# Optimization experiments

Hardware: AMD Instinct MI355X
Metric: run time of the kernel (lower is better)

## Reference

```python
import jax, jax.numpy as jnp
import numpy as np

N_NODES = 100000
N_EDGES = 1600000
F = 64          # node_features (in == out for EvolveGCNO)
HID = 64        # hidden_size


def setup_inputs() -> dict:
    key = jax.random.key(0)
    ks = jax.random.split(key, 12)
    s = 1.0 / np.sqrt(F)
    inp = {
        "x": jax.random.normal(ks[0], (N_NODES, F), dtype=jnp.float32),
        "edge_index": jax.random.randint(ks[1], (2, N_EDGES), 0, N_NODES, dtype=jnp.int64),
        "edge_weight": jax.random.uniform(ks[2], (N_EDGES,), dtype=jnp.float32),
        # evolving GCN weight (initial_weight of EvolveGCNO)
        "W0": jax.random.uniform(ks[3], (F, F), jnp.float32, -s, s),
        # GRU (input_size=F, hidden_size=F): gates ordered r, z, n
        "gru_Wi": jax.random.uniform(ks[4], (3 * F, F), jnp.float32, -s, s),
        "gru_Wh": jax.random.uniform(ks[5], (3 * F, F), jnp.float32, -s, s),
        "gru_bi": jax.random.uniform(ks[6], (3 * F,), jnp.float32, -s, s),
        "gru_bh": jax.random.uniform(ks[7], (3 * F,), jnp.float32, -s, s),
        # projection F -> HID and head HID -> 1
        "proj_W": jax.random.uniform(ks[8], (HID, F), jnp.float32, -s, s),
        "proj_b": jax.random.uniform(ks[9], (HID,), jnp.float32, -s, s),
        "lin_W": jax.random.uniform(ks[10], (1, HID), jnp.float32, -1.0 / np.sqrt(HID), 1.0 / np.sqrt(HID)),
        "lin_b": jax.random.uniform(ks[11], (1,), jnp.float32, -1.0 / np.sqrt(HID), 1.0 / np.sqrt(HID)),
    }
    return inp


def reference(x, edge_index, edge_weight, W0, gru_Wi, gru_Wh, gru_bi, gru_bh,
              proj_W, proj_b, lin_W, lin_b):
    N = x.shape[0]
    # --- EvolveGCNO weight evolution: one GRU step, rows of W0 are both input and hidden ---
    gi = W0 @ gru_Wi.T + gru_bi  # [F, 3F]
    gh = W0 @ gru_Wh.T + gru_bh  # [F, 3F]
    i_r, i_z, i_n = jnp.split(gi, 3, axis=1)
    h_r, h_z, h_n = jnp.split(gh, 3, axis=1)
    r = jax.nn.sigmoid(i_r + h_r)
    z = jax.nn.sigmoid(i_z + h_z)
    n = jnp.tanh(i_n + r * h_n)
    W = (1.0 - z) * n + z * W0  # evolved GCN weight [F, F]

    # --- GCNConv with fixed evolved W: X' = D^-1/2 (A + I) D^-1/2 (X W) ---
    xw = x @ W  # [N, F]
    src, dst = edge_index[0], edge_index[1]
    loop = jnp.arange(N)
    src2 = jnp.concatenate([src, loop])
    dst2 = jnp.concatenate([dst, loop])
    w2 = jnp.concatenate([edge_weight, jnp.ones((N,), xw.dtype)])  # self-loop weight 1
    deg = jax.ops.segment_sum(w2, dst2, num_segments=N)
    dinv = jnp.where(deg > 0, jax.lax.rsqrt(deg), 0.0)
    norm = dinv[src2] * w2 * dinv[dst2]  # [E + N]
    h = jax.ops.segment_sum(xw[src2] * norm[:, None], dst2, num_segments=N)  # [N, F]

    # --- MLP head (dropout is identity in eval) ---
    h = jax.nn.relu(h @ proj_W.T + proj_b)
    return h @ lin_W.T + lin_b  # [N, 1]
```

## Files before the change

### kernel.cpp

```cpp
#include <hip/hip_runtime.h>
#include <stdint.h>

#define FDIM 64
#define BINSH 6
#define NBINS 1563
#define BCAP 1536
#define OVCAP 8192
#define PSTAGE 8192

__device__ __forceinline__ float bf2f(unsigned int u) {
    union { float f; uint32_t i; } v; v.i = (u & 0xFFFFu) << 16; return v.f;
}
__device__ __forceinline__ unsigned short f2bf(float f) {
    union { float f; uint32_t i; } v; v.f = f;
    uint32_t u = v.i;
    u += 0x7FFFu + ((u >> 16) & 1u);
    return (unsigned short)(u >> 16);
}

__global__ __launch_bounds__(256) void k_sentinel(float* out, int N, float val) {
    int n = blockIdx.x * 256 + threadIdx.x;
    if (n < N) out[n] = (n == 0) ? val : 0.f;
}

__global__ __launch_bounds__(64) void k_evolveM(
    const float* __restrict__ W0, const float* __restrict__ Wi,
    const float* __restrict__ Wh, const float* __restrict__ bi,
    const float* __restrict__ bh, const float* __restrict__ projW,
    float* __restrict__ M, int* __restrict__ gcnt, int* __restrict__ ovf_cnt) {
    int i = blockIdx.x;
    int j = threadIdx.x;
    int g = i * 64 + j;
    if (g < NBINS) gcnt[g] = 0;
    if (g == NBINS) *ovf_cnt = 0;
    __shared__ float w0s[64];
    __shared__ float wrow[64];
    w0s[j] = W0[i * 64 + j];
    __syncthreads();
    float a0 = 0.f, a1 = 0.f, a2 = 0.f, b0 = 0.f, b1 = 0.f, b2 = 0.f;
#pragma unroll 8
    for (int k = 0; k < 64; k++) {
        float w0k = w0s[k];
        a0 += w0k * Wi[(j)       * 64 + k];
        a1 += w0k * Wi[(64 + j)  * 64 + k];
        a2 += w0k * Wi[(128 + j) * 64 + k];
        b0 += w0k * Wh[(j)       * 64 + k];
        b1 += w0k * Wh[(64 + j)  * 64 + k];
        b2 += w0k * Wh[(128 + j) * 64 + k];
    }
    float ir = a0 + bi[j],        hr = b0 + bh[j];
    float iz = a1 + bi[64 + j],   hz = b1 + bh[64 + j];
    float in_ = a2 + bi[128 + j], hn = b2 + bh[128 + j];
    float r = 1.f / (1.f + expf(-(ir + hr)));
    float z = 1.f / (1.f + expf(-(iz + hz)));
    float n = tanhf(in_ + r * hn);
    wrow[j] = (1.f - z) * n + z * w0s[j];
    __syncthreads();
    float s = 0.f;
#pragma unroll 8
    for (int q = 0; q < 64; q++) s += wrow[q] * projW[j * 64 + q];
    M[i * 64 + j] = s;
}

__global__ __launch_bounds__(256) void k_xm(
    const float* __restrict__ x, const float* __restrict__ M,
    unsigned short* __restrict__ xm, int N) {
    __shared__ float xs[64 * 68];
    __shared__ float ms[64 * 68];
    int t  = threadIdx.x;
    int nb = blockIdx.x * 64;
#pragma unroll
    for (int i = 0; i < 4; i++) {
        int lin = i * 1024 + t * 4;
        int row = lin >> 6, col = lin & 63;
        int node = nb + row;
        float4 v = make_float4(0.f, 0.f, 0.f, 0.f);
        if (node < N) v = *(const float4*)(x + (size_t)node * 64 + col);
        *(float4*)&xs[row * 68 + col] = v;
        *(float4*)&ms[row * 68 + col] = *(const float4*)(M + lin);
    }
    __syncthreads();
    int tj = t & 15, tn = t >> 4;
    float acc[4][4] = {};
    for (int k = 0; k < 64; k += 4) {
        float4 xv[4], mv[4];
#pragma unroll
        for (int nn = 0; nn < 4; nn++) xv[nn] = *(const float4*)&xs[(tn * 4 + nn) * 68 + k];
#pragma unroll
        for (int kk = 0; kk < 4; kk++) mv[kk] = *(const float4*)&ms[(k + kk) * 68 + tj * 4];
#pragma unroll
        for (int nn = 0; nn < 4; nn++) {
            const float* xp = (const float*)&xv[nn];
#pragma unroll
            for (int kk = 0; kk < 4; kk++) {
                float xk = xp[kk];
                const float* mp = (const float*)&mv[kk];
                acc[nn][0] += xk * mp[0];
                acc[nn][1] += xk * mp[1];
                acc[nn][2] += xk * mp[2];
                acc[nn][3] += xk * mp[3];
            }
        }
    }
#pragma unroll
    for (int nn = 0; nn < 4; nn++) {
        int node = nb + tn * 4 + nn;
        if (node < N) {
            ushort4 o;
            o.x = f2bf(acc[nn][0]); o.y = f2bf(acc[nn][1]);
            o.z = f2bf(acc[nn][2]); o.w = f2bf(acc[nn][3]);
            *(ushort4*)&xm[(size_t)node * 64 + tj * 4] = o;
        }
    }
}

__global__ __launch_bounds__(1024) void k_part(
    const int* __restrict__ src, const int* __restrict__ dst,
    const float* __restrict__ ew, int* __restrict__ gcnt,
    int2* __restrict__ part, int* __restrict__ ovf_cnt,
    int* __restrict__ ovs, int* __restrict__ ovd, float* __restrict__ ovw,
    int E) {
    __shared__ int hist[NBINS];
    __shared__ int lcur[NBINS];
    int t = threadIdx.x;
    for (int b = t; b < NBINS; b += 1024) hist[b] = 0;
    __syncthreads();
    int e0 = blockIdx.x * PSTAGE;
    int cnt = E - e0; if (cnt > PSTAGE) cnt = PSTAGE;
    for (int i = t; i < cnt; i += 1024) atomicAdd(&hist[dst[e0 + i] >> BINSH], 1);
    __syncthreads();
    for (int b = t; b < NBINS; b += 1024) {
        int h = hist[b];
        lcur[b] = h ? atomicAdd(&gcnt[b], h) : 0;
    }
    __syncthreads();
    for (int i = t; i < cnt; i += 1024) {
        int e = e0 + i;
        int d = dst[e];
        int b = d >> BINSH;
        int p = atomicAdd(&lcur[b], 1);
        if (p < BCAP) {
            part[(size_t)b * BCAP + p] = make_int2(src[e] | ((d & 63) << 20),
                                                   __float_as_int(ew[e]));
        } else {
            int op = atomicAdd(ovf_cnt, 1);
            if (op < OVCAP) {
                ovs[op] = src[e];
                ovd[op] = d;
                ovw[op] = ew[e];
            }
        }
    }
}

__global__ __launch_bounds__(256) void k_deg2(
    const int* __restrict__ gcnt, const int2* __restrict__ part,
    const int* __restrict__ ovf_cnt, const int* __restrict__ ovd,
    const float* __restrict__ ovw,
    float* __restrict__ deg, float* __restrict__ dinv, int N) {
    __shared__ float dl[64];
    int t = threadIdx.x, b = blockIdx.x;
    if (t < 64) dl[t] = 1.0f;
    __syncthreads();
    int c = gcnt[b]; if (c > BCAP) c = BCAP;
    const int2* pe = part + (size_t)b * BCAP;
    for (int i = t; i < c; i += 256) {
        int2 e = pe[i];
        atomicAdd(&dl[(e.x >> 20) & 63], __int_as_float(e.y));
    }
    int m = *ovf_cnt; if (m > OVCAP) m = OVCAP;
    for (int i = t; i < m; i += 256) {
        int d = ovd[i];
        if ((d >> BINSH) == b) atomicAdd(&dl[d & 63], ovw[i]);
    }
    __syncthreads();
    int n = b * 64 + t;
    if (t < 64 && n < N) {
        float d = dl[t];
        deg[n] = d;
        dinv[n] = d > 0.f ? rsqrtf(d) : 0.f;
    }
}

__global__ __launch_bounds__(256) void k_gf(
    const unsigned short* __restrict__ xm, const float* __restrict__ dinv,
    const int* __restrict__ gcnt, const int2* __restrict__ part,
    const float* __restrict__ projB, const float* __restrict__ linW,
    const float* __restrict__ linB, const int* __restrict__ ovf_cnt,
    const int* __restrict__ ovs, const int* __restrict__ ovd,
    const float* __restrict__ ovw, float* __restrict__ out, int N) {
    __shared__ int  lcnt[64];
    __shared__ int  loff[65];
    __shared__ int  lcur[64];
    __shared__ int2 ledge[BCAP];
    __shared__ float pbs[64], lws[64];
    int t = threadIdx.x, b = blockIdx.x;
    if (t < 64) { lcnt[t] = 0; pbs[t] = projB[t]; lws[t] = linW[t]; }
    __syncthreads();
    int c = gcnt[b]; if (c > BCAP) c = BCAP;
    const int2* pe = part + (size_t)b * BCAP;
    for (int i = t; i < c; i += 256) {
        atomicAdd(&lcnt[(pe[i].x >> 20) & 63], 1);
    }
    __syncthreads();
    if (t == 0) {
        int o = 0;
#pragma unroll 16
        for (int k = 0; k < 64; k++) { loff[k] = o; o += lcnt[k]; }
        loff[64] = o;
    }
    __syncthreads();
    if (t < 64) lcur[t] = loff[t];
    __syncthreads();
    for (int i = t; i < c; i += 256) {
        int2 e = pe[i];
        int s = e.x & 0xFFFFF;
        float nw = dinv[s] * __int_as_float(e.y);
        int p = atomicAdd(&lcur[(e.x >> 20) & 63], 1);
        ledge[p] = make_int2(e.x, __float_as_int(nw));
    }
    __syncthreads();
    int m = *ovf_cnt; if (m > OVCAP) m = OVCAP;
    float lb = linB[0];
    int wv = t >> 6, lane = t & 63, eg = lane >> 4, fq = lane & 15, f = fq * 4;
    for (int nl = wv; nl < 64; nl += 4) {
        int n = b * 64 + nl;
        if (n >= N) continue;
        float dn = dinv[n];
        int beg = loff[nl], end = loff[nl + 1];
        float ax = 0.f, ay = 0.f, az = 0.f, aw = 0.f;
        float bx = 0.f, by = 0.f, bz = 0.f, bw = 0.f;
        int i = beg + eg;
        for (; i + 4 < end; i += 8) {
            int2 e0 = ledge[i];
            int2 e1 = ledge[i + 4];
            int s0 = e0.x & 0xFFFFF, s1 = e1.x & 0xFFFFF;
            uint2 u0 = *(const uint2*)&xm[(size_t)s0 * 64 + f];
            uint2 u1 = *(const uint2*)&xm[(size_t)s1 * 64 + f];
            float nm0 = __int_as_float(e0.y);
            float nm1 = __int_as_float(e1.y);
            ax += nm0 * bf2f(u0.x);       ay += nm0 * bf2f(u0.x >> 16);
            az += nm0 * bf2f(u0.y);       aw += nm0 * bf2f(u0.y >> 16);
            bx += nm1 * bf2f(u1.x);       by += nm1 * bf2f(u1.x >> 16);
            bz += nm1 * bf2f(u1.y);       bw += nm1 * bf2f(u1.y >> 16);
        }
        for (; i < end; i += 4) {
            int2 e = ledge[i];
            int s = e.x & 0xFFFFF;
            float nm = __int_as_float(e.y);
            uint2 u = *(const uint2*)&xm[(size_t)s * 64 + f];
            ax += nm * bf2f(u.x); ay += nm * bf2f(u.x >> 16);
            az += nm * bf2f(u.y); aw += nm * bf2f(u.y >> 16);
        }
        ax += bx; ay += by; az += bz; aw += bw;
        ax *= dn; ay *= dn; az *= dn; aw *= dn;
        ax += __shfl_xor(ax, 16); ay += __shfl_xor(ay, 16);
        az += __shfl_xor(az, 16); aw += __shfl_xor(aw, 16);
        ax += __shfl_xor(ax, 32); ay += __shfl_xor(ay, 32);
        az += __shfl_xor(az, 32); aw += __shfl_xor(aw, 32);
        if (eg == 0) {
            {
                uint2 u = *(const uint2*)&xm[(size_t)n * 64 + f];
                float sl = dn * dn;
                ax += sl * bf2f(u.x); ay += sl * bf2f(u.x >> 16);
                az += sl * bf2f(u.y); aw += sl * bf2f(u.y >> 16);
            }
            for (int q = 0; q < m; q++) {
                if (ovd[q] == n) {
                    int s = ovs[q];
                    float nm = dinv[s] * ovw[q] * dn;
                    uint2 u = *(const uint2*)&xm[(size_t)s * 64 + f];
                    ax += nm * bf2f(u.x); ay += nm * bf2f(u.x >> 16);
                    az += nm * bf2f(u.y); aw += nm * bf2f(u.y >> 16);
                }
            }
            float v0 = ax + pbs[f],     v1 = ay + pbs[f + 1];
            float v2 = az + pbs[f + 2], v3 = aw + pbs[f + 3];
            float s = (v0 > 0.f ? v0 : 0.f) * lws[f]
                    + (v1 > 0.f ? v1 : 0.f) * lws[f + 1]
                    + (v2 > 0.f ? v2 : 0.f) * lws[f + 2]
                    + (v3 > 0.f ? v3 : 0.f) * lws[f + 3];
            s += __shfl_xor(s, 1); s += __shfl_xor(s, 2);
            s += __shfl_xor(s, 4); s += __shfl_xor(s, 8);
            if (fq == 0) out[n] = s + lb;
        }
    }
}

extern "C" void kernel_launch(void* const* d_in, const int* in_sizes, int n_in,
                              void* d_out, int out_size, void* d_ws, size_t ws_size,
                              hipStream_t stream) {
    const float* x   = (const float*)d_in[0];
    const int*   ei  = (const int*)d_in[1];
    const float* ew  = (const float*)d_in[2];
    const float* W0  = (const float*)d_in[3];
    const float* gWi = (const float*)d_in[4];
    const float* gWh = (const float*)d_in[5];
    const float* gbi = (const float*)d_in[6];
    const float* gbh = (const float*)d_in[7];
    const float* pW  = (const float*)d_in[8];
    const float* pb  = (const float*)d_in[9];
    const float* lW  = (const float*)d_in[10];
    const float* lb  = (const float*)d_in[11];
    float* out = (float*)d_out;

    static const int EXPSZ[12] = {6400000, 3200000, 1600000, 4096, 12288, 12288,
                                  192, 192, 4096, 64, 64, 1};
    int mism = -1;
    for (int i = 0; i < 12 && i < n_in; i++)
        if (in_sizes[i] != EXPSZ[i]) { mism = i; break; }
    if (mism >= 0) {
        k_sentinel<<<(out_size + 255) / 256, 256, 0, stream>>>(out, out_size,
                                                               ldexpf(1.f, 30 + 3 * mism));
        return;
    }

    int N = in_sizes[0] / FDIM;
    int E = in_sizes[1] / 2;
    const int* src = ei;
    const int* dst = ei + E;

    char* wsb = (char*)d_ws;
    float* M       = (float*)(wsb);
    int*   gcnt    = (int*)  (wsb + (32u << 10));
    int*   ovf_cnt = (int*)  (wsb + (39u << 10));
    int*   ovs     = (int*)  (wsb + (44u << 10));
    int*   ovd     = (int*)  (wsb + (76u << 10));
    float* ovw     = (float*)(wsb + (108u << 10));
    float* deg     = (float*)(wsb + (512u << 10));
    float* dinv    = (float*)(wsb + (1u << 20));
    int2*  part    = (int2*) (wsb + (2u << 20));
    unsigned short* xm = (unsigned short*)(wsb + (22u << 20));

    k_evolveM<<<64, 64, 0, stream>>>(W0, gWi, gWh, gbi, gbh, pW, M, gcnt, ovf_cnt);
    k_xm<<<NBINS, 256, 0, stream>>>(x, M, xm, N);
    k_part<<<(E + PSTAGE - 1) / PSTAGE, 1024, 0, stream>>>(src, dst, ew, gcnt, part,
                                                           ovf_cnt, ovs, ovd, ovw, E);
    k_deg2<<<NBINS, 256, 0, stream>>>(gcnt, part, ovf_cnt, ovd, ovw, deg, dinv, N);
    k_gf<<<NBINS, 256, 0, stream>>>(xm, dinv, gcnt, part, pb, lW, lb,
                                    ovf_cnt, ovs, ovd, ovw, out, N);
}
```

Before: 195.9 us.

## Merge independent kernels into shared launches and precompute per-node edge offsets

Edge partitioning and the GRU weight evolution now run as disjoint block ranges of one launch. The x@M bf16 projection and the degree pass share a second launch the same way. The degree pass also counts edges per node and writes the prefix offsets to global memory, so the gather kernel no longer runs its own histogram and scan. A memset replaces the in-kernel counter zeroing. This cuts five launches down to a memset plus three and removes redundant partition reads, but k_prep's evolve blocks now carry 1024-thread blocks with most threads idle.

After: 193.4 us. No clear change (-1.3%).

```diff
diff --git a/kernel.cpp b/kernel.cpp
--- a/kernel.cpp
+++ b/kernel.cpp
@@ -7,6 +7,8 @@
 #define BCAP 1536
 #define OVCAP 8192
 #define PSTAGE 8192
+#define PBLK 196
+#define LSTRIDE 72
 
 __device__ __forceinline__ float bf2f(unsigned int u) {
     union { float f; uint32_t i; } v; v.i = (u & 0xFFFFu) << 16; return v.f;
@@ -23,195 +25,197 @@
     if (n < N) out[n] = (n == 0) ? val : 0.f;
 }
 
-__global__ __launch_bounds__(64) void k_evolveM(
+__global__ __launch_bounds__(1024) void k_prep(
+    const int* __restrict__ src, const int* __restrict__ dst,
+    const float* __restrict__ ew, int* __restrict__ gcnt,
+    int2* __restrict__ part, int* __restrict__ ovf_cnt,
+    int* __restrict__ ovs, int* __restrict__ ovd, float* __restrict__ ovw, int E,
     const float* __restrict__ W0, const float* __restrict__ Wi,
     const float* __restrict__ Wh, const float* __restrict__ bi,
     const float* __restrict__ bh, const float* __restrict__ projW,
-    float* __restrict__ M, int* __restrict__ gcnt, int* __restrict__ ovf_cnt) {
-    int i = blockIdx.x;
-    int j = threadIdx.x;
-    int g = i * 64 + j;
-    if (g < NBINS) gcnt[g] = 0;
-    if (g == NBINS) *ovf_cnt = 0;
-    __shared__ float w0s[64];
-    __shared__ float wrow[64];
-    w0s[j] = W0[i * 64 + j];
-    __syncthreads();
-    float a0 = 0.f, a1 = 0.f, a2 = 0.f, b0 = 0.f, b1 = 0.f, b2 = 0.f;
+    float* __restrict__ M) {
+    __shared__ char sm[12504];
+    int t = threadIdx.x;
+    if (blockIdx.x < PBLK) {
+        int* hist = (int*)sm;
+        int* lcur = hist + NBINS;
+        for (int b = t; b < NBINS; b += 1024) hist[b] = 0;
+        __syncthreads();
+        int e0 = blockIdx.x * PSTAGE;
+        int cnt = E - e0; if (cnt > PSTAGE) cnt = PSTAGE;
+        for (int i = t; i < cnt; i += 1024) atomicAdd(&hist[dst[e0 + i] >> BINSH], 1);
+        __syncthreads();
+        for (int b = t; b < NBINS; b += 1024) {
+            int h = hist[b];
+            lcur[b] = h ? atomicAdd(&gcnt[b], h) : 0;
+        }
+        __syncthreads();
+        for (int i = t; i < cnt; i += 1024) {
+            int e = e0 + i;
+            int d = dst[e];
+            int b = d >> BINSH;
+            int p = atomicAdd(&lcur[b], 1);
+            if (p < BCAP) {
+                part[(size_t)b * BCAP + p] = make_int2(src[e] | ((d & 63) << 20),
+                                                       __float_as_int(ew[e]));
+            } else {
+                int op = atomicAdd(ovf_cnt, 1);
+                if (op < OVCAP) {
+                    ovs[op] = src[e];
+                    ovd[op] = d;
+                    ovw[op] = ew[e];
+                }
+            }
+        }
+    } else {
+        int i = blockIdx.x - PBLK;
+        float* w0s  = (float*)sm;
+        float* wrow = w0s + 64;
+        if (t < 64) w0s[t] = W0[i * 64 + t];
+        __syncthreads();
+        if (t < 64) {
+            int j = t;
+            float a0 = 0.f, a1 = 0.f, a2 = 0.f, b0 = 0.f, b1 = 0.f, b2 = 0.f;
 #pragma unroll 8
-    for (int k = 0; k < 64; k++) {
-        float w0k = w0s[k];
-        a0 += w0k * Wi[(j)       * 64 + k];
-        a1 += w0k * Wi[(64 + j)  * 64 + k];
-        a2 += w0k * Wi[(128 + j) * 64 + k];
-        b0 += w0k * Wh[(j)       * 64 + k];
-        b1 += w0k * Wh[(64 + j)  * 64 + k];
-        b2 += w0k * Wh[(128 + j) * 64 + k];
-    }
-    float ir = a0 + bi[j],        hr = b0 + bh[j];
-    float iz = a1 + bi[64 + j],   hz = b1 + bh[64 + j];
-    float in_ = a2 + bi[128 + j], hn = b2 + bh[128 + j];
-    float r = 1.f / (1.f + expf(-(ir + hr)));
-    float z = 1.f / (1.f + expf(-(iz + hz)));
-    float n = tanhf(in_ + r * hn);
-    wrow[j] = (1.f - z) * n + z * w0s[j];
-    __syncthreads();
-    float s = 0.f;
+            for (int k = 0; k < 64; k++) {
+                float w0k = w0s[k];
+                a0 += w0k * Wi[(j)       * 64 + k];
+                a1 += w0k * Wi[(64 + j)  * 64 + k];
+                a2 += w0k * Wi[(128 + j) * 64 + k];
+                b0 += w0k * Wh[(j)       * 64 + k];
+                b1 += w0k * Wh[(64 + j)  * 64 + k];
+                b2 += w0k * Wh[(128 + j) * 64 + k];
+            }
+            float ir = a0 + bi[j],        hr = b0 + bh[j];
+            float iz = a1 + bi[64 + j],   hz = b1 + bh[64 + j];
+            float in_ = a2 + bi[128 + j], hn = b2 + bh[128 + j];
+            float r = 1.f / (1.f + expf(-(ir + hr)));
+            float z = 1.f / (1.f + expf(-(iz + hz)));
+            float n = tanhf(in_ + r * hn);
+            wrow[j] = (1.f - z) * n + z * w0s[j];
+        }
+        __syncthreads();
+        if (t < 64) {
+            float s = 0.f;
 #pragma unroll 8
-    for (int q = 0; q < 64; q++) s += wrow[q] * projW[j * 64 + q];
-    M[i * 64 + j] = s;
-}
-
-__global__ __launch_bounds__(256) void k_xm(
+            for (int q = 0; q < 64; q++) s += wrow[q] * projW[t * 64 + q];
+            M[i * 64 + t] = s;
+        }
+    }
+}
+
+__global__ __launch_bounds__(256) void k_xmdeg(
     const float* __restrict__ x, const float* __restrict__ M,
-    unsigned short* __restrict__ xm, int N) {
-    __shared__ float xs[64 * 68];
-    __shared__ float ms[64 * 68];
-    int t  = threadIdx.x;
-    int nb = blockIdx.x * 64;
-#pragma unroll
-    for (int i = 0; i < 4; i++) {
-        int lin = i * 1024 + t * 4;
-        int row = lin >> 6, col = lin & 63;
-        int node = nb + row;
-        float4 v = make_float4(0.f, 0.f, 0.f, 0.f);
-        if (node < N) v = *(const float4*)(x + (size_t)node * 64 + col);
-        *(float4*)&xs[row * 68 + col] = v;
-        *(float4*)&ms[row * 68 + col] = *(const float4*)(M + lin);
-    }
-    __syncthreads();
-    int tj = t & 15, tn = t >> 4;
-    float acc[4][4] = {};
-    for (int k = 0; k < 64; k += 4) {
-        float4 xv[4], mv[4];
-#pragma unroll
-        for (int nn = 0; nn < 4; nn++) xv[nn] = *(const float4*)&xs[(tn * 4 + nn) * 68 + k];
-#pragma unroll
-        for (int kk = 0; kk < 4; kk++) mv[kk] = *(const float4*)&ms[(k + kk) * 68 + tj * 4];
-#pragma unroll
-        for (int nn = 0; nn < 4; nn++) {
-            const float* xp = (const float*)&xv[nn];
-#pragma unroll
-            for (int kk = 0; kk < 4; kk++) {
-                float xk = xp[kk];
-                const float* mp = (const float*)&mv[kk];
-                acc[nn][0] += xk * mp[0];
-                acc[nn][1] += xk * mp[1];
-                acc[nn][2] += xk * mp[2];
-                acc[nn][3] += xk * mp[3];
-            }
-        }
-    }
-#pragma unroll
-    for (int nn = 0; nn < 4; nn++) {
-        int node = nb + tn * 4 + nn;
-        if (node < N) {
-            ushort4 o;
-            o.x = f2bf(acc[nn][0]); o.y = f2bf(acc[nn][1]);
-            o.z = f2bf(acc[nn][2]); o.w = f2bf(acc[nn][3]);
-            *(ushort4*)&xm[(size_t)node * 64 + tj * 4] = o;
-        }
-    }
-}
-
-__global__ __launch_bounds__(1024) void k_part(
-    const int* __restrict__ src, const int* __restrict__ dst,
-    const float* __restrict__ ew, int* __restrict__ gcnt,
-    int2* __restrict__ part, int* __restrict__ ovf_cnt,
-    int* __restrict__ ovs, int* __restrict__ ovd, float* __restrict__ ovw,
-    int E) {
-    __shared__ int hist[NBINS];
-    __shared__ int lcur[NBINS];
-    int t = threadIdx.x;
-    for (int b = t; b < NBINS; b += 1024) hist[b] = 0;
-    __syncthreads();
-    int e0 = blockIdx.x * PSTAGE;
-    int cnt = E - e0; if (cnt > PSTAGE) cnt = PSTAGE;
-    for (int i = t; i < cnt; i += 1024) atomicAdd(&hist[dst[e0 + i] >> BINSH], 1);
-    __syncthreads();
-    for (int b = t; b < NBINS; b += 1024) {
-        int h = hist[b];
-        lcur[b] = h ? atomicAdd(&gcnt[b], h) : 0;
-    }
-    __syncthreads();
-    for (int i = t; i < cnt; i += 1024) {
-        int e = e0 + i;
-        int d = dst[e];
-        int b = d >> BINSH;
-        int p = atomicAdd(&lcur[b], 1);
-        if (p < BCAP) {
-            part[(size_t)b * BCAP + p] = make_int2(src[e] | ((d & 63) << 20),
-                                                   __float_as_int(ew[e]));
-        } else {
-            int op = atomicAdd(ovf_cnt, 1);
-            if (op < OVCAP) {
-                ovs[op] = src[e];
-                ovd[op] = d;
-                ovw[op] = ew[e];
-            }
-        }
-    }
-}
-
-__global__ __launch_bounds__(256) void k_deg2(
+    unsigned short* __restrict__ xm, int N,
     const int* __restrict__ gcnt, const int2* __restrict__ part,
     const int* __restrict__ ovf_cnt, const int* __restrict__ ovd,
-    const float* __restrict__ ovw,
-    float* __restrict__ deg, float* __restrict__ dinv, int N) {
-    __shared__ float dl[64];
-    int t = threadIdx.x, b = blockIdx.x;
-    if (t < 64) dl[t] = 1.0f;
-    __syncthreads();
-    int c = gcnt[b]; if (c > BCAP) c = BCAP;
-    const int2* pe = part + (size_t)b * BCAP;
-    for (int i = t; i < c; i += 256) {
-        int2 e = pe[i];
-        atomicAdd(&dl[(e.x >> 20) & 63], __int_as_float(e.y));
-    }
-    int m = *ovf_cnt; if (m > OVCAP) m = OVCAP;
-    for (int i = t; i < m; i += 256) {
-        int d = ovd[i];
-        if ((d >> BINSH) == b) atomicAdd(&dl[d & 63], ovw[i]);
-    }
-    __syncthreads();
-    int n = b * 64 + t;
-    if (t < 64 && n < N) {
-        float d = dl[t];
-        deg[n] = d;
-        dinv[n] = d > 0.f ? rsqrtf(d) : 0.f;
+    const float* __restrict__ ovw, float* __restrict__ dinv,
+    int* __restrict__ loffg) {
+    __shared__ char sm[34816];
+    int t = threadIdx.x;
+    if (blockIdx.x < NBINS) {
+        float* xs = (float*)sm;
+        float* ms = xs + 64 * 68;
+        int nb = blockIdx.x * 64;
+#pragma unroll
+        for (int i = 0; i < 4; i++) {
+            int lin = i * 1024 + t * 4;
+            int row = lin >> 6, col = lin & 63;
+            int node = nb + row;
+            float4 v = make_float4(0.f, 0.f, 0.f, 0.f);
+            if (node < N) v = *(const float4*)(x + (size_t)node * 64 + col);
+            *(float4*)&xs[row * 68 + col] = v;
+            *(float4*)&ms[row * 68 + col] = *(const float4*)(M + lin);
+        }
+        __syncthreads();
+        int tj = t & 15, tn = t >> 4;
+        float acc[4][4] = {};
+        for (int k = 0; k < 64; k += 4) {
+            float4 xv[4], mv[4];
+#pragma unroll
+            for (int nn = 0; nn < 4; nn++) xv[nn] = *(const float4*)&xs[(tn * 4 + nn) * 68 + k];
+#pragma unroll
+            for (int kk = 0; kk < 4; kk++) mv[kk] = *(const float4*)&ms[(k + kk) * 68 + tj * 4];
+#pragma unroll
+            for (int nn = 0; nn < 4; nn++) {
+                const float* xp = (const float*)&xv[nn];
+#pragma unroll
+                for (int kk = 0; kk < 4; kk++) {
+                    float xk = xp[kk];
+                    const float* mp = (const float*)&mv[kk];
+                    acc[nn][0] += xk * mp[0];
+                    acc[nn][1] += xk * mp[1];
+                    acc[nn][2] += xk * mp[2];
+                    acc[nn][3] += xk * mp[3];
+                }
+            }
+        }
+#pragma unroll
+        for (int nn = 0; nn < 4; nn++) {
+            int node = nb + tn * 4 + nn;
+            if (node < N) {
+                ushort4 o;
+                o.x = f2bf(acc[nn][0]); o.y = f2bf(acc[nn][1]);
+                o.z = f2bf(acc[nn][2]); o.w = f2bf(acc[nn][3]);
+                *(ushort4*)&xm[(size_t)node * 64 + tj * 4] = o;
+            }
+        }
+    } else {
+        int b = blockIdx.x - NBINS;
+        float* dl   = (float*)sm;
+        int*   cntl = (int*)(dl + 64);
+        int*   lofl = cntl + 64;
+        if (t < 64) { dl[t] = 1.0f; cntl[t] = 0; }
+        __syncthreads();
+        int c = gcnt[b]; if (c > BCAP) c = BCAP;
+        const int2* pe = part + (size_t)b * BCAP;
+        for (int i = t; i < c; i += 256) {
+            int2 e = pe[i];
+            int nl = (e.x >> 20) & 63;
+            atomicAdd(&dl[nl], __int_as_float(e.y));
+            atomicAdd(&cntl[nl], 1);
+        }
+        int m = *ovf_cnt; if (m > OVCAP) m = OVCAP;
+        for (int i = t; i < m; i += 256) {
+            int d = ovd[i];
+            if ((d >> BINSH) == b) atomicAdd(&dl[d & 63], ovw[i]);
+        }
+        __syncthreads();
+        if (t == 0) {
+            int o = 0;
+#pragma unroll 16
+            for (int k = 0; k < 64; k++) { lofl[k] = o; o += cntl[k]; }
+            lofl[64] = o;
+        }
+        __syncthreads();
+        if (t < 64) {
+            int n = b * 64 + t;
+            if (n < N) dinv[n] = rsqrtf(dl[t]);
+        }
+        if (t < 65) loffg[b * LSTRIDE + t] = lofl[t];
     }
 }
 
 __global__ __launch_bounds__(256) void k_gf(
     const unsigned short* __restrict__ xm, const float* __restrict__ dinv,
     const int* __restrict__ gcnt, const int2* __restrict__ part,
+    const int* __restrict__ loffg,
     const float* __restrict__ projB, const float* __restrict__ linW,
     const float* __restrict__ linB, const int* __restrict__ ovf_cnt,
     const int* __restrict__ ovs, const int* __restrict__ ovd,
     const float* __restrict__ ovw, float* __restrict__ out, int N) {
-    __shared__ int  lcnt[64];
     __shared__ int  loff[65];
     __shared__ int  lcur[64];
     __shared__ int2 ledge[BCAP];
     __shared__ float pbs[64], lws[64];
     int t = threadIdx.x, b = blockIdx.x;
-    if (t < 64) { lcnt[t] = 0; pbs[t] = projB[t]; lws[t] = linW[t]; }
+    if (t < 65) loff[t] = loffg[b * LSTRIDE + t];
+    if (t < 64) { pbs[t] = projB[t]; lws[t] = linW[t]; }
+    __syncthreads();
+    if (t < 64) lcur[t] = loff[t];
     __syncthreads();
     int c = gcnt[b]; if (c > BCAP) c = BCAP;
     const int2* pe = part + (size_t)b * BCAP;
-    for (int i = t; i < c; i += 256) {
-        atomicAdd(&lcnt[(pe[i].x >> 20) & 63], 1);
-    }
-    __syncthreads();
-    if (t == 0) {
-        int o = 0;
-#pragma unroll 16
-        for (int k = 0; k < 64; k++) { loff[k] = o; o += lcnt[k]; }
-        loff[64] = o;
-    }
-    __syncthreads();
-    if (t < 64) lcur[t] = loff[t];
-    __syncthreads();
     for (int i = t; i < c; i += 256) {
         int2 e = pe[i];
         int s = e.x & 0xFFFFF;
@@ -327,16 +331,18 @@
     int*   ovs     = (int*)  (wsb + (44u << 10));
     int*   ovd     = (int*)  (wsb + (76u << 10));
     float* ovw     = (float*)(wsb + (108u << 10));
-    float* deg     = (float*)(wsb + (512u << 10));
     float* dinv    = (float*)(wsb + (1u << 20));
+    int*   loffg   = (int*)  (wsb + 1572864u);
     int2*  part    = (int2*) (wsb + (2u << 20));
     unsigned short* xm = (unsigned short*)(wsb + (22u << 20));
 
-    k_evolveM<<<64, 64, 0, stream>>>(W0, gWi, gWh, gbi, gbh, pW, M, gcnt, ovf_cnt);
-    k_xm<<<NBINS, 256, 0, stream>>>(x, M, xm, N);
-    k_part<<<(E + PSTAGE - 1) / PSTAGE, 1024, 0, stream>>>(src, dst, ew, gcnt, part,
-                                                           ovf_cnt, ovs, ovd, ovw, E);
-    k_deg2<<<NBINS, 256, 0, stream>>>(gcnt, part, ovf_cnt, ovd, ovw, deg, dinv, N);
-    k_gf<<<NBINS, 256, 0, stream>>>(xm, dinv, gcnt, part, pb, lW, lb,
+    hipMemsetAsync(gcnt, 0, (8u << 10), stream);
+
+    k_prep<<<PBLK + 64, 1024, 0, stream>>>(src, dst, ew, gcnt, part,
+                                           ovf_cnt, ovs, ovd, ovw, E,
+                                           W0, gWi, gWh, gbi, gbh, pW, M);
+    k_xmdeg<<<NBINS * 2, 256, 0, stream>>>(x, M, xm, N, gcnt, part,
+                                           ovf_cnt, ovd, ovw, dinv, loffg);
+    k_gf<<<NBINS, 256, 0, stream>>>(xm, dinv, gcnt, part, loffg, pb, lW, lb,
                                     ovf_cnt, ovs, ovd, ovw, out, N);
 }
```
